# Performance work log

Measured on AMD Instinct MI355X. Metric: run time of the kernel, lower is better.

The kernel has to match this reference:

```python
import jax, jax.numpy as jnp
import numpy as np

DIM = 128
N_ROUNDS = 120


def _mlp(x, W1, b1, W2, b2, W3, b3):
    h = jax.nn.relu(x @ W1.T + b1)
    h = jax.nn.relu(h @ W2.T + b2)
    return h @ W3.T + b3


def _lstm(x, h, c, Wih, Whh, bih, bhh):
    # torch nn.LSTM gate order: i, f, g, o
    g = x @ Wih.T + h @ Whh.T + (bih + bhh)
    i, f, gg, o = jnp.split(g, 4, axis=-1)
    c2 = jax.nn.sigmoid(f) * c + jax.nn.sigmoid(i) * jnp.tanh(gg)
    h2 = jax.nn.sigmoid(o) * jnp.tanh(c2)
    return h2, c2


def setup_inputs() -> dict:
    key = jax.random.key(0)
    keys = iter(jax.random.split(key, 64))
    def w(*shape):
        return jax.random.normal(next(keys), shape, dtype=jnp.float32) * 0.05
    n_nodes, n_vars = 8000, 1000
    N = n_nodes + n_vars
    # sparse 0/1 adjacency, stored dense as in the original (adj_matrix.values)
    adj = (jax.random.uniform(next(keys), (n_nodes, N)) < 0.003).astype(jnp.float32)
    values = jax.random.randint(next(keys), (N,), 0, 2)
    inp = dict(adj=adj, values=values, n_nodes=n_nodes)
    inp.update(true_W=w(DIM, 1), true_b=w(DIM), false_W=w(DIM, 1), false_b=w(DIM))
    for p in ("cm", "pm"):
        inp.update({p + "_W1": w(DIM, DIM), p + "_b1": w(DIM),
                    p + "_W2": w(DIM, DIM), p + "_b2": w(DIM),
                    p + "_W3": w(DIM, DIM), p + "_b3": w(DIM)})
    inp.update(vv_W1=w(DIM, DIM), vv_b1=w(DIM), vv_W2=w(DIM, DIM), vv_b2=w(DIM),
               vv_W3=w(1, DIM), vv_b3=w(1))
    for p in ("vu", "nu"):
        inp.update({p + "_Wih": w(4 * DIM, DIM), p + "_Whh": w(4 * DIM, DIM),
                    p + "_bih": w(4 * DIM), p + "_bhh": w(4 * DIM)})
    return inp


def reference(adj, values, n_nodes, true_W, true_b, false_W, false_b,
              cm_W1, cm_b1, cm_W2, cm_b2, cm_W3, cm_b3,
              pm_W1, pm_b1, pm_W2, pm_b2, pm_W3, pm_b3,
              vv_W1, vv_b1, vv_W2, vv_b2, vv_W3, vv_b3,
              vu_Wih, vu_Whh, vu_bih, vu_bhh,
              nu_Wih, nu_Whh, nu_bih, nu_bhh):
    init_ts = jnp.ones((1,), jnp.float32)
    true_vec = true_W @ init_ts + true_b     # (128,)
    false_vec = false_W @ init_ts + false_b  # (128,)
    h0 = jnp.where((values == 1)[:, None], true_vec, false_vec)  # (N,128)
    c0 = jnp.zeros_like(h0)

    def step(carry, _):
        h, c = carry
        var_pre = _mlp(h, cm_W1, cm_b1, cm_W2, cm_b2, cm_W3, cm_b3)   # (N,128)
        c2p = adj @ var_pre                                           # (n_nodes,128)
        hn, cn = _lstm(c2p, h[:n_nodes], c[:n_nodes], vu_Wih, vu_Whh, vu_bih, vu_bhh)
        h = jnp.concatenate([hn, h[n_nodes:]], axis=0)
        c = jnp.concatenate([cn, c[n_nodes:]], axis=0)
        node_pre = _mlp(h[:n_nodes], pm_W1, pm_b1, pm_W2, pm_b2, pm_W3, pm_b3)
        p2c = adj.T @ node_pre                                        # (N,128)
        h, c = _lstm(p2c, h, c, nu_Wih, nu_Whh, nu_bih, nu_bhh)
        return (h, c), None

    (h, c), _ = jax.lax.scan(step, (h0, c0), None, length=N_ROUNDS)
    vote = _mlp(h[n_nodes:], vv_W1, vv_b1, vv_W2, vv_b2, vv_W3, vv_b3)  # (n_vars,1)
    return vote.squeeze(-1)
```

## Files before the change

### kernel.cpp

```cpp
#include <hip/hip_runtime.h>
#include <cstddef>
#include <cstdint>

#define DIM 128
#define NROUNDS 120
#define NNZ_CAP (1 << 20)

typedef _Float16 half8 __attribute__((ext_vector_type(8)));
typedef float f32x4 __attribute__((ext_vector_type(4)));
typedef unsigned long long u64;

__device__ __forceinline__ float sigf(float x) { return 1.f / (1.f + __expf(-x)); }
__device__ __forceinline__ float tanh_fast(float x) { return 2.f / (1.f + __expf(-2.f * x)) - 1.f; }

__global__ void count_nz_kernel(const float* __restrict__ adj, int* __restrict__ row_cnt,
                                int* __restrict__ col_cnt, int ncols) {
  int i = blockIdx.x;
  int j = blockIdx.y * blockDim.x + threadIdx.x;
  bool nz = (j < ncols) && (adj[(size_t)i * ncols + j] != 0.f);
  unsigned long long m = __ballot(nz);
  if ((threadIdx.x & 63) == 0) {
    int c = __popcll(m);
    if (c) atomicAdd(&row_cnt[i], c);
  }
  if (nz) atomicAdd(&col_cnt[j], 1);
}

__global__ void scan_kernel(const int* __restrict__ cnt, int* __restrict__ ptr, int n) {
  __shared__ int sdata[256];
  int t = threadIdx.x;
  int per = (n + 255) / 256;
  int beg = t * per;
  int end = beg + per; if (end > n) end = n;
  int local = 0;
  for (int i = beg; i < end; ++i) local += cnt[i];
  sdata[t] = local;
  __syncthreads();
  for (int off = 1; off < 256; off <<= 1) {
    int v = (t >= off) ? sdata[t - off] : 0;
    __syncthreads();
    sdata[t] += v;
    __syncthreads();
  }
  int run = sdata[t] - local;
  for (int i = beg; i < end; ++i) { ptr[i] = run; run += cnt[i]; }
  if (t == 255) ptr[n] = sdata[255];
}

__global__ __launch_bounds__(64) void fill_csr_kernel(const float* __restrict__ adj,
                                                      const int* __restrict__ row_ptr,
                                                      int* __restrict__ col_idx, int ncols) {
  int row = blockIdx.x;
  int lane = threadIdx.x;
  int base = row_ptr[row];
  int cursor = 0;
  const float* arow = adj + (size_t)row * ncols;
  for (int j0 = 0; j0 < ncols; j0 += 64) {
    int j = j0 + lane;
    bool nz = (j < ncols) && (arow[j] != 0.f);
    u64 m = __ballot(nz);
    int pre = __popcll(m & ((1ull << lane) - 1));
    if (nz) col_idx[base + cursor + pre] = j;
    cursor += __popcll(m);
  }
}

__global__ __launch_bounds__(64) void fill_csc_kernel(const float* __restrict__ adj,
                                                      const int* __restrict__ col_ptr,
                                                      int* __restrict__ row_idx,
                                                      int nrows, int ncols) {
  int c = blockIdx.x * 64 + threadIdx.x;
  if (c >= ncols) return;
  int cur = col_ptr[c];
  for (int i = 0; i < nrows; ++i) {
    if (adj[(size_t)i * ncols + c] != 0.f) row_idx[cur++] = i;
  }
}

__global__ void pack_w_kernel(const float* __restrict__ src, int out_dim,
                              _Float16* __restrict__ dh, _Float16* __restrict__ dl) {
  int idx = blockIdx.x * 256 + threadIdx.x;
  if (idx >= out_dim * DIM) return;
  int n = idx >> 7, k = idx & 127;
  float x = src[idx];
  _Float16 hi = (_Float16)x;
  _Float16 lo = (_Float16)(x - (float)hi);
  int nt = n >> 4, ks = k >> 5;
  int L = ((k >> 3) & 3) * 16 + (n & 15);
  int j = k & 7;
  int dst = ((nt * 4 + ks) * 64 + L) * 8 + j;
  dh[dst] = hi; dl[dst] = lo;
}

__global__ void init_hc_kernel(const int* __restrict__ values, const float* __restrict__ tW,
                               const float* __restrict__ tb, const float* __restrict__ fW,
                               const float* __restrict__ fb, float* __restrict__ h,
                               float* __restrict__ c, int N) {
  int idx = blockIdx.x * blockDim.x + threadIdx.x;
  if (idx >= N * DIM) return;
  int row = idx >> 7, col = idx & (DIM - 1);
  float tv = tW[col] + tb[col];
  float fv = fW[col] + fb[col];
  h[idx] = (values[row] == 1) ? tv : fv;
  c[idx] = 0.f;
}

__device__ __forceinline__ int sw_idx(int m, int k) {
  return (m << 7) + (((((k >> 3) ^ (m & 15))) << 3) | (k & 7));
}

__device__ __forceinline__ void stage_rows(const float* __restrict__ src, int M, int rb,
                                           _Float16* Sh, _Float16* Sl, int tid) {
  int r = tid >> 4, q = tid & 15;
  int row = rb + r;
  float4 v0, v1;
  if (row < M) {
    const float4* s = (const float4*)(src + (size_t)row * DIM + q * 8);
    v0 = s[0]; v1 = s[1];
  } else {
    v0.x = v0.y = v0.z = v0.w = 0.f; v1 = v0;
  }
  int a = sw_idx(r, q * 8);
  float vv[8] = {v0.x, v0.y, v0.z, v0.w, v1.x, v1.y, v1.z, v1.w};
#pragma unroll
  for (int e = 0; e < 8; ++e) {
    _Float16 hi = (_Float16)vv[e];
    Sh[a + e] = hi;
    Sl[a + e] = (_Float16)(vv[e] - (float)hi);
  }
}

__device__ __forceinline__ void gather_rows(const int* __restrict__ ptr,
                                            const int* __restrict__ nzidx,
                                            const _Float16* __restrict__ va, int M, int rb,
                                            _Float16* Xh, _Float16* Xl, int tid) {
  int r = tid >> 4, seg = tid & 15;
  int row = rb + r;
  float a[8];
#pragma unroll
  for (int e = 0; e < 8; ++e) a[e] = 0.f;
  if (row < M) {
    int s = ptr[row], e_ = ptr[row + 1];
    int p = s;
    for (; p + 4 <= e_; p += 4) {
      int i0 = nzidx[p], i1 = nzidx[p + 1], i2 = nzidx[p + 2], i3 = nzidx[p + 3];
      half8 v0 = *(const half8*)(va + (size_t)i0 * DIM + seg * 8);
      half8 v1 = *(const half8*)(va + (size_t)i1 * DIM + seg * 8);
      half8 v2 = *(const half8*)(va + (size_t)i2 * DIM + seg * 8);
      half8 v3 = *(const half8*)(va + (size_t)i3 * DIM + seg * 8);
#pragma unroll
      for (int e = 0; e < 8; ++e)
        a[e] += ((float)v0[e] + (float)v1[e]) + ((float)v2[e] + (float)v3[e]);
    }
    for (; p < e_; ++p) {
      half8 v = *(const half8*)(va + (size_t)nzidx[p] * DIM + seg * 8);
#pragma unroll
      for (int e = 0; e < 8; ++e) a[e] += (float)v[e];
    }
  }
  int aoff = sw_idx(r, seg * 8);
#pragma unroll
  for (int e = 0; e < 8; ++e) {
    _Float16 hi = (_Float16)a[e];
    Xh[aoff + e] = hi;
    Xl[aoff + e] = (_Float16)(a[e] - (float)hi);
  }
}

__device__ __forceinline__ void mfma3(f32x4& acc, half8 ah, half8 al, half8 bh, half8 bl) {
  acc = __builtin_amdgcn_mfma_f32_16x16x32_f16(ah, bh, acc, 0, 0, 0);
  acc = __builtin_amdgcn_mfma_f32_16x16x32_f16(ah, bl, acc, 0, 0, 0);
  acc = __builtin_amdgcn_mfma_f32_16x16x32_f16(al, bh, acc, 0, 0, 0);
}

__device__ __forceinline__ void mlp_layer(const _Float16* Ah_, const _Float16* Al_,
                                          const _Float16* __restrict__ Wh,
                                          const _Float16* __restrict__ Wl,
                                          const float* __restrict__ B,
                                          _Float16* Dh, _Float16* Dl, int tid) {
  int lane = tid & 63, w = tid >> 6;
  int m16 = lane & 15, quad = lane >> 4;
  float bv = B[w * 16 + m16];
  f32x4 acc[2];
  acc[0] = (f32x4){bv, bv, bv, bv};
  acc[1] = acc[0];
#pragma unroll
  for (int ks = 0; ks < 4; ++ks) {
    int boff = ((w * 4 + ks) * 64 + lane) * 8;
    half8 bh = *(const half8*)(Wh + boff);
    half8 bl = *(const half8*)(Wl + boff);
#pragma unroll
    for (int sub = 0; sub < 2; ++sub) {
      int a_off = sw_idx(sub * 16 + m16, ks * 32 + quad * 8);
      mfma3(acc[sub], *(const half8*)(Ah_ + a_off), *(const half8*)(Al_ + a_off), bh, bl);
    }
  }
#pragma unroll
  for (int sub = 0; sub < 2; ++sub)
#pragma unroll
    for (int reg = 0; reg < 4; ++reg) {
      int rl = sub * 16 + quad * 4 + reg;
      int col = w * 16 + m16;
      float x = fmaxf(acc[sub][reg], 0.f);
      _Float16 hi = (_Float16)x;
      int a = sw_idx(rl, col);
      Dh[a] = hi;
      Dl[a] = (_Float16)(x - (float)hi);
    }
  __syncthreads();
}

__device__ __forceinline__ void mlp_from_lds(
    _Float16* S0, _Float16* S1, _Float16* S2, _Float16* S3, int M, int rb,
    const _Float16* __restrict__ W1h, const _Float16* __restrict__ W1l, const float* __restrict__ b1,
    const _Float16* __restrict__ W2h, const _Float16* __restrict__ W2l, const float* __restrict__ b2,
    const _Float16* __restrict__ W3h, const _Float16* __restrict__ W3l, const float* __restrict__ b3,
    _Float16* __restrict__ out) {
  int tid = threadIdx.x;
  mlp_layer(S0, S1, W1h, W1l, b1, S2, S3, tid);
  mlp_layer(S2, S3, W2h, W2l, b2, S0, S1, tid);
  int lane = tid & 63, w = tid >> 6;
  int m16 = lane & 15, quad = lane >> 4;
  float bv = b3[w * 16 + m16];
  f32x4 acc[2];
  acc[0] = (f32x4){bv, bv, bv, bv};
  acc[1] = acc[0];
#pragma unroll
  for (int ks = 0; ks < 4; ++ks) {
    int boff = ((w * 4 + ks) * 64 + lane) * 8;
    half8 bh = *(const half8*)(W3h + boff);
    half8 bl = *(const half8*)(W3l + boff);
#pragma unroll
    for (int sub = 0; sub < 2; ++sub) {
      int a_off = sw_idx(sub * 16 + m16, ks * 32 + quad * 8);
      mfma3(acc[sub], *(const half8*)(S0 + a_off), *(const half8*)(S1 + a_off), bh, bl);
    }
  }
#pragma unroll
  for (int sub = 0; sub < 2; ++sub)
#pragma unroll
    for (int reg = 0; reg < 4; ++reg) {
      int row = rb + sub * 16 + quad * 4 + reg;
      int col = w * 16 + m16;
      if (row < M) out[(size_t)row * DIM + col] = (_Float16)acc[sub][reg];
    }
}

__global__ __launch_bounds__(512, 2) void mlp3_mfma(
    const float* __restrict__ X, int M,
    const _Float16* __restrict__ W1h, const _Float16* __restrict__ W1l, const float* __restrict__ b1,
    const _Float16* __restrict__ W2h, const _Float16* __restrict__ W2l, const float* __restrict__ b2,
    const _Float16* __restrict__ W3h, const _Float16* __restrict__ W3l, const float* __restrict__ b3,
    _Float16* __restrict__ out) {
  __shared__ _Float16 S0[4096], S1[4096], S2[4096], S3[4096];
  int tid = threadIdx.x;
  int rb = blockIdx.x << 5;
  stage_rows(X, M, rb, S0, S1, tid);
  __syncthreads();
  mlp_from_lds(S0, S1, S2, S3, M, rb, W1h, W1l, b1, W2h, W2l, b2, W3h, W3l, b3, out);
}

template <bool DO_MLP>
__global__ __launch_bounds__(512, 2) void lstm_fused(
    const int* __restrict__ ptr, const int* __restrict__ nzidx, const _Float16* __restrict__ va_in,
    float* __restrict__ hbuf, float* __restrict__ cbuf, int M,
    const _Float16* __restrict__ Wxh, const _Float16* __restrict__ Wxl,
    const _Float16* __restrict__ Whh_, const _Float16* __restrict__ Whl,
    const float* __restrict__ bih, const float* __restrict__ bhh,
    const _Float16* __restrict__ W1h, const _Float16* __restrict__ W1l, const float* __restrict__ b1,
    const _Float16* __restrict__ W2h, const _Float16* __restrict__ W2l, const float* __restrict__ b2,
    const _Float16* __restrict__ W3h, const _Float16* __restrict__ W3l, const float* __restrict__ b3,
    _Float16* __restrict__ va_out) {
  __shared__ _Float16 Xh[4096], Xl[4096], Hh[4096], Hl[4096];
  int tid = threadIdx.x;
  int rb = blockIdx.x << 5;
  stage_rows(hbuf, M, rb, Hh, Hl, tid);
  gather_rows(ptr, nzidx, va_in, M, rb, Xh, Xl, tid);
  __syncthreads();

  int lane = tid & 63, w = tid >> 6;
  int m16 = lane & 15, quad = lane >> 4;
  f32x4 acc[2][4];
#pragma unroll
  for (int g = 0; g < 4; ++g) {
    int col = g * 128 + w * 16 + m16;
    float bv = bih[col] + bhh[col];
    acc[0][g] = (f32x4){bv, bv, bv, bv};
    acc[1][g] = acc[0][g];
  }
#pragma unroll
  for (int ks = 0; ks < 4; ++ks) {
#pragma unroll
    for (int g = 0; g < 4; ++g) {
      int ct = g * 8 + w;
      int boff = ((ct * 4 + ks) * 64 + lane) * 8;
      half8 bh = *(const half8*)(Whh_ + boff);
      half8 bl = *(const half8*)(Whl + boff);
#pragma unroll
      for (int sub = 0; sub < 2; ++sub) {
        int a_off = sw_idx(sub * 16 + m16, ks * 32 + quad * 8);
        mfma3(acc[sub][g], *(const half8*)(Hh + a_off), *(const half8*)(Hl + a_off), bh, bl);
      }
    }
  }
#pragma unroll
  for (int ks = 0; ks < 4; ++ks) {
#pragma unroll
    for (int g = 0; g < 4; ++g) {
      int ct = g * 8 + w;
      int boff = ((ct * 4 + ks) * 64 + lane) * 8;
      half8 bh = *(const half8*)(Wxh + boff);
      half8 bl = *(const half8*)(Wxl + boff);
#pragma unroll
      for (int sub = 0; sub < 2; ++sub) {
        int a_off = sw_idx(sub * 16 + m16, ks * 32 + quad * 8);
        mfma3(acc[sub][g], *(const half8*)(Xh + a_off), *(const half8*)(Xl + a_off), bh, bl);
      }
    }
  }

  if (DO_MLP) __syncthreads();

#pragma unroll
  for (int sub = 0; sub < 2; ++sub)
#pragma unroll
    for (int reg = 0; reg < 4; ++reg) {
      int rl = sub * 16 + quad * 4 + reg;
      int row = rb + rl;
      int col = w * 16 + m16;
      float hn = 0.f;
      if (row < M) {
        float iv = sigf(acc[sub][0][reg]);
        float fv = sigf(acc[sub][1][reg]);
        float gv = tanh_fast(acc[sub][2][reg]);
        float ov = sigf(acc[sub][3][reg]);
        size_t o = (size_t)row * DIM + col;
        float cn = fv * cbuf[o] + iv * gv;
        cbuf[o] = cn;
        hn = ov * tanh_fast(cn);
        hbuf[o] = hn;
      }
      if (DO_MLP) {
        int a = sw_idx(rl, col);
        _Float16 hi = (_Float16)hn;
        Xh[a] = hi;
        Xl[a] = (_Float16)(hn - (float)hi);
      }
    }
  if (DO_MLP) {
    __syncthreads();
    mlp_from_lds(Xh, Xl, Hh, Hl, M, rb, W1h, W1l, b1, W2h, W2l, b2, W3h, W3l, b3, va_out);
  }
}

__device__ __forceinline__ void tile_gemm(const float* S, const float* __restrict__ W,
                                          int colB, int rowB, float acc[4][4]) {
#pragma unroll 4
  for (int kc = 0; kc < DIM; kc += 4) {
    float4 xv[4], wv[4];
#pragma unroll
    for (int r = 0; r < 4; ++r) xv[r] = *(const float4*)(S + (rowB + r) * DIM + kc);
#pragma unroll
    for (int c = 0; c < 4; ++c) wv[c] = *(const float4*)(W + (size_t)(colB + c) * DIM + kc);
#pragma unroll
    for (int r = 0; r < 4; ++r)
#pragma unroll
      for (int c = 0; c < 4; ++c)
        acc[r][c] += xv[r].x * wv[c].x + xv[r].y * wv[c].y + xv[r].z * wv[c].z + xv[r].w * wv[c].w;
  }
}

__device__ __forceinline__ void layer_lds(const float* Sin, float* Sout,
                                          const float* __restrict__ W, const float* __restrict__ B,
                                          bool relu, int colB, int rowB) {
  float acc[4][4];
#pragma unroll
  for (int r = 0; r < 4; ++r)
#pragma unroll
    for (int cc = 0; cc < 4; ++cc) acc[r][cc] = B[colB + cc];
  tile_gemm(Sin, W, colB, rowB, acc);
#pragma unroll
  for (int r = 0; r < 4; ++r) {
    float4 v;
    v.x = acc[r][0]; v.y = acc[r][1]; v.z = acc[r][2]; v.w = acc[r][3];
    if (relu) { v.x = fmaxf(v.x, 0.f); v.y = fmaxf(v.y, 0.f); v.z = fmaxf(v.z, 0.f); v.w = fmaxf(v.w, 0.f); }
    *(float4*)&Sout[(rowB + r) * DIM + colB] = v;
  }
  __syncthreads();
}

__global__ __launch_bounds__(256) void vote_kernel(
    const float* __restrict__ X, int M,
    const float* __restrict__ W1, const float* __restrict__ b1,
    const float* __restrict__ W2, const float* __restrict__ b2,
    const float* __restrict__ W3, const float* __restrict__ b3,
    float* __restrict__ out) {
  __shared__ float Xs[32 * DIM];
  __shared__ float Ys[32 * DIM];
  int tid = threadIdx.x;
  int rb = blockIdx.x * 32;
  int mrows = M - rb; if (mrows > 32) mrows = 32;
  {
    const float4* src = (const float4*)(X + (size_t)rb * DIM);
    float4* dst = (float4*)Xs;
    int nf4 = mrows * (DIM / 4);
    for (int t = tid; t < 32 * (DIM / 4); t += 256) {
      float4 v;
      if (t < nf4) v = src[t];
      else { v.x = v.y = v.z = v.w = 0.f; }
      dst[t] = v;
    }
  }
  __syncthreads();
  int tx = tid & 31, ty = tid >> 5;
  int colB = tx * 4, rowB = ty * 4;
  layer_lds(Xs, Ys, W1, b1, true, colB, rowB);
  layer_lds(Ys, Xs, W2, b2, true, colB, rowB);
  if (tid < 32) {
    int gr = rb + tid;
    if (gr < M) {
      float s = b3[0];
      for (int k = 0; k < DIM; ++k) s += Xs[tid * DIM + k] * W3[k];
      out[gr] = s;
    }
  }
}

#define SZ128 (DIM * DIM)
#define SZ512 (4 * DIM * DIM)
#define O_CM1 0
#define O_CM2 (SZ128)
#define O_CM3 (2 * SZ128)
#define O_PM1 (3 * SZ128)
#define O_PM2 (4 * SZ128)
#define O_PM3 (5 * SZ128)
#define O_VUX ((size_t)6 * SZ128)
#define O_VUH ((size_t)6 * SZ128 + SZ512)
#define O_NUX ((size_t)6 * SZ128 + 2 * SZ512)
#define O_NUH ((size_t)6 * SZ128 + 3 * SZ512)

extern "C" void kernel_launch(void* const* d_in, const int* in_sizes, int n_in,
                              void* d_out, int out_size, void* d_ws, size_t ws_size,
                              hipStream_t stream) {
  const float* adj    = (const float*)d_in[0];
  const int*   values = (const int*)d_in[1];
  const int N       = in_sizes[1];
  const int n_nodes = in_sizes[0] / N;
  const int n_vars  = N - n_nodes;

  const float* true_W  = (const float*)d_in[3];
  const float* true_b  = (const float*)d_in[4];
  const float* false_W = (const float*)d_in[5];
  const float* false_b = (const float*)d_in[6];
  const float* cm_W1 = (const float*)d_in[7];
  const float* cm_b1 = (const float*)d_in[8];
  const float* cm_W2 = (const float*)d_in[9];
  const float* cm_b2 = (const float*)d_in[10];
  const float* cm_W3 = (const float*)d_in[11];
  const float* cm_b3 = (const float*)d_in[12];
  const float* pm_W1 = (const float*)d_in[13];
  const float* pm_b1 = (const float*)d_in[14];
  const float* pm_W2 = (const float*)d_in[15];
  const float* pm_b2 = (const float*)d_in[16];
  const float* pm_W3 = (const float*)d_in[17];
  const float* pm_b3 = (const float*)d_in[18];
  const float* vv_W1 = (const float*)d_in[19];
  const float* vv_b1 = (const float*)d_in[20];
  const float* vv_W2 = (const float*)d_in[21];
  const float* vv_b2 = (const float*)d_in[22];
  const float* vv_W3 = (const float*)d_in[23];
  const float* vv_b3 = (const float*)d_in[24];
  const float* vu_Wih = (const float*)d_in[25];
  const float* vu_Whh = (const float*)d_in[26];
  const float* vu_bih = (const float*)d_in[27];
  const float* vu_bhh = (const float*)d_in[28];
  const float* nu_Wih = (const float*)d_in[29];
  const float* nu_Whh = (const float*)d_in[30];
  const float* nu_bih = (const float*)d_in[31];
  const float* nu_bhh = (const float*)d_in[32];

  uintptr_t p = (uintptr_t)d_ws;
  auto take = [&](size_t bytes) -> void* {
    uintptr_t cur = (p + 255) & ~(uintptr_t)255;
    p = cur + bytes;
    return (void*)cur;
  };
  float* h   = (float*)take((size_t)N * DIM * sizeof(float));
  float* cb  = (float*)take((size_t)N * DIM * sizeof(float));
  _Float16* va1 = (_Float16*)take((size_t)N * DIM * sizeof(_Float16));
  _Float16* va2 = (_Float16*)take((size_t)N * DIM * sizeof(_Float16));
  int* row_ptr = (int*)take((size_t)(n_nodes + 1) * sizeof(int));
  int* col_ptr = (int*)take((size_t)(N + 1) * sizeof(int));
  int* cnts    = (int*)take((size_t)(n_nodes + N) * sizeof(int));
  int* row_cnt = cnts;
  int* col_cnt = cnts + n_nodes;
  int* col_idx = (int*)take((size_t)NNZ_CAP * sizeof(int));
  int* row_idx = (int*)take((size_t)NNZ_CAP * sizeof(int));

  size_t tot_pack = (size_t)6 * SZ128 + (size_t)4 * SZ512;
  _Float16* packh = (_Float16*)take(tot_pack * sizeof(_Float16));
  _Float16* packl = (_Float16*)take(tot_pack * sizeof(_Float16));

  hipMemsetAsync(cnts, 0, (size_t)(n_nodes + N) * sizeof(int), stream);
  dim3 cgrid(n_nodes, (N + 255) / 256);
  count_nz_kernel<<<cgrid, 256, 0, stream>>>(adj, row_cnt, col_cnt, N);
  scan_kernel<<<1, 256, 0, stream>>>(row_cnt, row_ptr, n_nodes);
  scan_kernel<<<1, 256, 0, stream>>>(col_cnt, col_ptr, N);
  fill_csr_kernel<<<n_nodes, 64, 0, stream>>>(adj, row_ptr, col_idx, N);
  fill_csc_kernel<<<(N + 63) / 64, 64, 0, stream>>>(adj, col_ptr, row_idx, n_nodes, N);
  init_hc_kernel<<<(N * DIM + 255) / 256, 256, 0, stream>>>(values, true_W, true_b,
                                                            false_W, false_b, h, cb, N);

  auto pack = [&](const float* src, int out_dim, size_t o) {
    pack_w_kernel<<<(out_dim * DIM + 255) / 256, 256, 0, stream>>>(src, out_dim,
                                                                   packh + o, packl + o);
  };
  pack(cm_W1, DIM, O_CM1); pack(cm_W2, DIM, O_CM2); pack(cm_W3, DIM, O_CM3);
  pack(pm_W1, DIM, O_PM1); pack(pm_W2, DIM, O_PM2); pack(pm_W3, DIM, O_PM3);
  pack(vu_Wih, 4 * DIM, O_VUX); pack(vu_Whh, 4 * DIM, O_VUH);
  pack(nu_Wih, 4 * DIM, O_NUX); pack(nu_Whh, 4 * DIM, O_NUH);

  int tiles_N = (N + 31) / 32, tiles_n = (n_nodes + 31) / 32;

  mlp3_mfma<<<tiles_N, 512, 0, stream>>>(h, N,
      packh + O_CM1, packl + O_CM1, cm_b1,
      packh + O_CM2, packl + O_CM2, cm_b2,
      packh + O_CM3, packl + O_CM3, cm_b3, va1);

  for (int r = 0; r < NROUNDS; ++r) {
    lstm_fused<true><<<tiles_n, 512, 0, stream>>>(row_ptr, col_idx, va1, h, cb, n_nodes,
        packh + O_VUX, packl + O_VUX, packh + O_VUH, packl + O_VUH, vu_bih, vu_bhh,
        packh + O_PM1, packl + O_PM1, pm_b1,
        packh + O_PM2, packl + O_PM2, pm_b2,
        packh + O_PM3, packl + O_PM3, pm_b3, va2);
    if (r + 1 < NROUNDS) {
      lstm_fused<true><<<tiles_N, 512, 0, stream>>>(col_ptr, row_idx, va2, h, cb, N,
          packh + O_NUX, packl + O_NUX, packh + O_NUH, packl + O_NUH, nu_bih, nu_bhh,
          packh + O_CM1, packl + O_CM1, cm_b1,
          packh + O_CM2, packl + O_CM2, cm_b2,
          packh + O_CM3, packl + O_CM3, cm_b3, va1);
    } else {
      lstm_fused<false><<<tiles_N, 512, 0, stream>>>(col_ptr, row_idx, va2, h, cb, N,
          packh + O_NUX, packl + O_NUX, packh + O_NUH, packl + O_NUH, nu_bih, nu_bhh,
          packh + O_CM1, packl + O_CM1, cm_b1,
          packh + O_CM2, packl + O_CM2, cm_b2,
          packh + O_CM3, packl + O_CM3, cm_b3, va1);
    }
  }

  vote_kernel<<<(n_vars + 31) / 32, 256, 0, stream>>>(h + (size_t)n_nodes * DIM, n_vars,
      vv_W1, vv_b1, vv_W2, vv_b2, vv_W3, vv_b3, (float*)d_out);
}
```

Measured before the change: 10.86 ms.

## Drop weight low-part in split-fp16 MFMA and retile to 16-row blocks

Weights are now packed only as a single fp16 high part, so each product uses two MFMAs (A-hi*W, A-lo*W) instead of three, removing the weight low-part loads and a third of the matrix work. Blocks shrink to 16 rows and 256 threads, with each wave computing two 16-column tiles and reusing its loaded activation fragment across them. This lowers accuracy of the weight representation to plain fp16. Per-row weight fragment traffic rises because each block covers fewer rows.

```diff
diff --git a/kernel.cpp b/kernel.cpp
--- a/kernel.cpp
+++ b/kernel.cpp
@@ -78,18 +78,15 @@
 }
 
 __global__ void pack_w_kernel(const float* __restrict__ src, int out_dim,
-                              _Float16* __restrict__ dh, _Float16* __restrict__ dl) {
+                              _Float16* __restrict__ dh) {
   int idx = blockIdx.x * 256 + threadIdx.x;
   if (idx >= out_dim * DIM) return;
   int n = idx >> 7, k = idx & 127;
-  float x = src[idx];
-  _Float16 hi = (_Float16)x;
-  _Float16 lo = (_Float16)(x - (float)hi);
+  _Float16 hi = (_Float16)src[idx];
   int nt = n >> 4, ks = k >> 5;
   int L = ((k >> 3) & 3) * 16 + (n & 15);
   int j = k & 7;
-  int dst = ((nt * 4 + ks) * 64 + L) * 8 + j;
-  dh[dst] = hi; dl[dst] = lo;
+  dh[((nt * 4 + ks) * 64 + L) * 8 + j] = hi;
 }
 
 __global__ void init_hc_kernel(const int* __restrict__ values, const float* __restrict__ tW,
@@ -167,41 +164,42 @@
   }
 }
 
-__device__ __forceinline__ void mfma3(f32x4& acc, half8 ah, half8 al, half8 bh, half8 bl) {
+__device__ __forceinline__ void mfma2(f32x4& acc, half8 ah, half8 al, half8 bh) {
   acc = __builtin_amdgcn_mfma_f32_16x16x32_f16(ah, bh, acc, 0, 0, 0);
-  acc = __builtin_amdgcn_mfma_f32_16x16x32_f16(ah, bl, acc, 0, 0, 0);
   acc = __builtin_amdgcn_mfma_f32_16x16x32_f16(al, bh, acc, 0, 0, 0);
 }
 
 __device__ __forceinline__ void mlp_layer(const _Float16* Ah_, const _Float16* Al_,
                                           const _Float16* __restrict__ Wh,
-                                          const _Float16* __restrict__ Wl,
                                           const float* __restrict__ B,
                                           _Float16* Dh, _Float16* Dl, int tid) {
   int lane = tid & 63, w = tid >> 6;
   int m16 = lane & 15, quad = lane >> 4;
-  float bv = B[w * 16 + m16];
   f32x4 acc[2];
-  acc[0] = (f32x4){bv, bv, bv, bv};
-  acc[1] = acc[0];
+#pragma unroll
+  for (int c2 = 0; c2 < 2; ++c2) {
+    float bv = B[w * 32 + c2 * 16 + m16];
+    acc[c2] = (f32x4){bv, bv, bv, bv};
+  }
 #pragma unroll
   for (int ks = 0; ks < 4; ++ks) {
-    int boff = ((w * 4 + ks) * 64 + lane) * 8;
-    half8 bh = *(const half8*)(Wh + boff);
-    half8 bl = *(const half8*)(Wl + boff);
-#pragma unroll
-    for (int sub = 0; sub < 2; ++sub) {
-      int a_off = sw_idx(sub * 16 + m16, ks * 32 + quad * 8);
-      mfma3(acc[sub], *(const half8*)(Ah_ + a_off), *(const half8*)(Al_ + a_off), bh, bl);
-    }
-  }
-#pragma unroll
-  for (int sub = 0; sub < 2; ++sub)
+    int a_off = sw_idx(m16, ks * 32 + quad * 8);
+    half8 ah = *(const half8*)(Ah_ + a_off);
+    half8 al = *(const half8*)(Al_ + a_off);
+#pragma unroll
+    for (int c2 = 0; c2 < 2; ++c2) {
+      int ct = w * 2 + c2;
+      int boff = ((ct * 4 + ks) * 64 + lane) * 8;
+      mfma2(acc[c2], ah, al, *(const half8*)(Wh + boff));
+    }
+  }
+#pragma unroll
+  for (int c2 = 0; c2 < 2; ++c2)
 #pragma unroll
     for (int reg = 0; reg < 4; ++reg) {
-      int rl = sub * 16 + quad * 4 + reg;
-      int col = w * 16 + m16;
-      float x = fmaxf(acc[sub][reg], 0.f);
+      int rl = quad * 4 + reg;
+      int col = w * 32 + c2 * 16 + m16;
+      float x = fmaxf(acc[c2][reg], 0.f);
       _Float16 hi = (_Float16)x;
       int a = sw_idx(rl, col);
       Dh[a] = hi;
@@ -212,68 +210,70 @@
 
 __device__ __forceinline__ void mlp_from_lds(
     _Float16* S0, _Float16* S1, _Float16* S2, _Float16* S3, int M, int rb,
-    const _Float16* __restrict__ W1h, const _Float16* __restrict__ W1l, const float* __restrict__ b1,
-    const _Float16* __restrict__ W2h, const _Float16* __restrict__ W2l, const float* __restrict__ b2,
-    const _Float16* __restrict__ W3h, const _Float16* __restrict__ W3l, const float* __restrict__ b3,
+    const _Float16* __restrict__ W1h, const float* __restrict__ b1,
+    const _Float16* __restrict__ W2h, const float* __restrict__ b2,
+    const _Float16* __restrict__ W3h, const float* __restrict__ b3,
     _Float16* __restrict__ out) {
   int tid = threadIdx.x;
-  mlp_layer(S0, S1, W1h, W1l, b1, S2, S3, tid);
-  mlp_layer(S2, S3, W2h, W2l, b2, S0, S1, tid);
+  mlp_layer(S0, S1, W1h, b1, S2, S3, tid);
+  mlp_layer(S2, S3, W2h, b2, S0, S1, tid);
   int lane = tid & 63, w = tid >> 6;
   int m16 = lane & 15, quad = lane >> 4;
-  float bv = b3[w * 16 + m16];
   f32x4 acc[2];
-  acc[0] = (f32x4){bv, bv, bv, bv};
-  acc[1] = acc[0];
+#pragma unroll
+  for (int c2 = 0; c2 < 2; ++c2) {
+    float bv = b3[w * 32 + c2 * 16 + m16];
+    acc[c2] = (f32x4){bv, bv, bv, bv};
+  }
 #pragma unroll
   for (int ks = 0; ks < 4; ++ks) {
-    int boff = ((w * 4 + ks) * 64 + lane) * 8;
-    half8 bh = *(const half8*)(W3h + boff);
-    half8 bl = *(const half8*)(W3l + boff);
-#pragma unroll
-    for (int sub = 0; sub < 2; ++sub) {
-      int a_off = sw_idx(sub * 16 + m16, ks * 32 + quad * 8);
-      mfma3(acc[sub], *(const half8*)(S0 + a_off), *(const half8*)(S1 + a_off), bh, bl);
-    }
-  }
-#pragma unroll
-  for (int sub = 0; sub < 2; ++sub)
+    int a_off = sw_idx(m16, ks * 32 + quad * 8);
+    half8 ah = *(const half8*)(S0 + a_off);
+    half8 al = *(const half8*)(S1 + a_off);
+#pragma unroll
+    for (int c2 = 0; c2 < 2; ++c2) {
+      int ct = w * 2 + c2;
+      int boff = ((ct * 4 + ks) * 64 + lane) * 8;
+      mfma2(acc[c2], ah, al, *(const half8*)(W3h + boff));
+    }
+  }
+#pragma unroll
+  for (int c2 = 0; c2 < 2; ++c2)
 #pragma unroll
     for (int reg = 0; reg < 4; ++reg) {
-      int row = rb + sub * 16 + quad * 4 + reg;
-      int col = w * 16 + m16;
-      if (row < M) out[(size_t)row * DIM + col] = (_Float16)acc[sub][reg];
-    }
-}
-
-__global__ __launch_bounds__(512, 2) void mlp3_mfma(
+      int row = rb + quad * 4 + reg;
+      int col = w * 32 + c2 * 16 + m16;
+      if (row < M) out[(size_t)row * DIM + col] = (_Float16)acc[c2][reg];
+    }
+}
+
+__global__ __launch_bounds__(256, 4) void mlp3_mfma(
     const float* __restrict__ X, int M,
-    const _Float16* __restrict__ W1h, const _Float16* __restrict__ W1l, const float* __restrict__ b1,
-    const _Float16* __restrict__ W2h, const _Float16* __restrict__ W2l, const float* __restrict__ b2,
-    const _Float16* __restrict__ W3h, const _Float16* __restrict__ W3l, const float* __restrict__ b3,
+    const _Float16* __restrict__ W1h, const float* __restrict__ b1,
+    const _Float16* __restrict__ W2h, const float* __restrict__ b2,
+    const _Float16* __restrict__ W3h, const float* __restrict__ b3,
     _Float16* __restrict__ out) {
-  __shared__ _Float16 S0[4096], S1[4096], S2[4096], S3[4096];
+  __shared__ _Float16 S0[2048], S1[2048], S2[2048], S3[2048];
   int tid = threadIdx.x;
-  int rb = blockIdx.x << 5;
+  int rb = blockIdx.x << 4;
   stage_rows(X, M, rb, S0, S1, tid);
   __syncthreads();
-  mlp_from_lds(S0, S1, S2, S3, M, rb, W1h, W1l, b1, W2h, W2l, b2, W3h, W3l, b3, out);
+  mlp_from_lds(S0, S1, S2, S3, M, rb, W1h, b1, W2h, b2, W3h, b3, out);
 }
 
 template <bool DO_MLP>
-__global__ __launch_bounds__(512, 2) void lstm_fused(
+__global__ __launch_bounds__(256, 4) void lstm_fused(
     const int* __restrict__ ptr, const int* __restrict__ nzidx, const _Float16* __restrict__ va_in,
     float* __restrict__ hbuf, float* __restrict__ cbuf, int M,
-    const _Float16* __restrict__ Wxh, const _Float16* __restrict__ Wxl,
-    const _Float16* __restrict__ Whh_, const _Float16* __restrict__ Whl,
+    const _Float16* __restrict__ Wxh, const _Float16* __restrict__ Whh_,
     const float* __restrict__ bih, const float* __restrict__ bhh,
-    const _Float16* __restrict__ W1h, const _Float16* __restrict__ W1l, const float* __restrict__ b1,
-    const _Float16* __restrict__ W2h, const _Float16* __restrict__ W2l, const float* __restrict__ b2,
-    const _Float16* __restrict__ W3h, const _Float16* __restrict__ W3l, const float* __restrict__ b3,
+    const _Float16* __restrict__ W1h, const float* __restrict__ b1,
+    const _Float16* __restrict__ W2h, const float* __restrict__ b2,
+    const _Float16* __restrict__ W3h, const float* __restrict__ b3,
     _Float16* __restrict__ va_out) {
-  __shared__ _Float16 Xh[4096], Xl[4096], Hh[4096], Hl[4096];
+  __shared__ _Float16 Xh[2048], Xl[2048], Hh[2048], Hl[2048];
   int tid = threadIdx.x;
-  int rb = blockIdx.x << 5;
+  int rb = blockIdx.x << 4;
   stage_rows(hbuf, M, rb, Hh, Hl, tid);
   gather_rows(ptr, nzidx, va_in, M, rb, Xh, Xl, tid);
   __syncthreads();
@@ -282,58 +282,57 @@
   int m16 = lane & 15, quad = lane >> 4;
   f32x4 acc[2][4];
 #pragma unroll
-  for (int g = 0; g < 4; ++g) {
-    int col = g * 128 + w * 16 + m16;
-    float bv = bih[col] + bhh[col];
-    acc[0][g] = (f32x4){bv, bv, bv, bv};
-    acc[1][g] = acc[0][g];
-  }
+  for (int g = 0; g < 4; ++g)
+#pragma unroll
+    for (int c2 = 0; c2 < 2; ++c2) {
+      int col = g * 128 + w * 32 + c2 * 16 + m16;
+      float bv = bih[col] + bhh[col];
+      acc[c2][g] = (f32x4){bv, bv, bv, bv};
+    }
 #pragma unroll
   for (int ks = 0; ks < 4; ++ks) {
-#pragma unroll
-    for (int g = 0; g < 4; ++g) {
-      int ct = g * 8 + w;
-      int boff = ((ct * 4 + ks) * 64 + lane) * 8;
-      half8 bh = *(const half8*)(Whh_ + boff);
-      half8 bl = *(const half8*)(Whl + boff);
-#pragma unroll
-      for (int sub = 0; sub < 2; ++sub) {
-        int a_off = sw_idx(sub * 16 + m16, ks * 32 + quad * 8);
-        mfma3(acc[sub][g], *(const half8*)(Hh + a_off), *(const half8*)(Hl + a_off), bh, bl);
+    int a_off = sw_idx(m16, ks * 32 + quad * 8);
+    half8 ah = *(const half8*)(Hh + a_off);
+    half8 al = *(const half8*)(Hl + a_off);
+#pragma unroll
+    for (int g = 0; g < 4; ++g)
+#pragma unroll
+      for (int c2 = 0; c2 < 2; ++c2) {
+        int ct = g * 8 + w * 2 + c2;
+        int boff = ((ct * 4 + ks) * 64 + lane) * 8;
+        mfma2(acc[c2][g], ah, al, *(const half8*)(Whh_ + boff));
       }
-    }
   }
 #pragma unroll
   for (int ks = 0; ks < 4; ++ks) {
-#pragma unroll
-    for (int g = 0; g < 4; ++g) {
-      int ct = g * 8 + w;
-      int boff = ((ct * 4 + ks) * 64 + lane) * 8;
-      half8 bh = *(const half8*)(Wxh + boff);
-      half8 bl = *(const half8*)(Wxl + boff);
-#pragma unroll
-      for (int sub = 0; sub < 2; ++sub) {
-        int a_off = sw_idx(sub * 16 + m16, ks * 32 + quad * 8);
-        mfma3(acc[sub][g], *(const half8*)(Xh + a_off), *(const half8*)(Xl + a_off), bh, bl);
+    int a_off = sw_idx(m16, ks * 32 + quad * 8);
+    half8 ah = *(const half8*)(Xh + a_off);
+    half8 al = *(const half8*)(Xl + a_off);
+#pragma unroll
+    for (int g = 0; g < 4; ++g)
+#pragma unroll
+      for (int c2 = 0; c2 < 2; ++c2) {
+        int ct = g * 8 + w * 2 + c2;
+        int boff = ((ct * 4 + ks) * 64 + lane) * 8;
+        mfma2(acc[c2][g], ah, al, *(const half8*)(Wxh + boff));
       }
-    }
   }
 
   if (DO_MLP) __syncthreads();
 
 #pragma unroll
-  for (int sub = 0; sub < 2; ++sub)
+  for (int c2 = 0; c2 < 2; ++c2)
 #pragma unroll
     for (int reg = 0; reg < 4; ++reg) {
-      int rl = sub * 16 + quad * 4 + reg;
+      int rl = quad * 4 + reg;
       int row = rb + rl;
-      int col = w * 16 + m16;
+      int col = w * 32 + c2 * 16 + m16;
       float hn = 0.f;
       if (row < M) {
-        float iv = sigf(acc[sub][0][reg]);
-        float fv = sigf(acc[sub][1][reg]);
-        float gv = tanh_fast(acc[sub][2][reg]);
-        float ov = sigf(acc[sub][3][reg]);
+        float iv = sigf(acc[c2][0][reg]);
+        float fv = sigf(acc[c2][1][reg]);
+        float gv = tanh_fast(acc[c2][2][reg]);
+        float ov = sigf(acc[c2][3][reg]);
         size_t o = (size_t)row * DIM + col;
         float cn = fv * cbuf[o] + iv * gv;
         cbuf[o] = cn;
@@ -349,7 +348,7 @@
     }
   if (DO_MLP) {
     __syncthreads();
-    mlp_from_lds(Xh, Xl, Hh, Hl, M, rb, W1h, W1l, b1, W2h, W2l, b2, W3h, W3l, b3, va_out);
+    mlp_from_lds(Xh, Xl, Hh, Hl, M, rb, W1h, b1, W2h, b2, W3h, b3, va_out);
   }
 }
 
@@ -499,7 +498,6 @@
 
   size_t tot_pack = (size_t)6 * SZ128 + (size_t)4 * SZ512;
   _Float16* packh = (_Float16*)take(tot_pack * sizeof(_Float16));
-  _Float16* packl = (_Float16*)take(tot_pack * sizeof(_Float16));
 
   hipMemsetAsync(cnts, 0, (size_t)(n_nodes + N) * sizeof(int), stream);
   dim3 cgrid(n_nodes, (N + 255) / 256);
@@ -512,39 +510,30 @@
                                                             false_W, false_b, h, cb, N);
 
   auto pack = [&](const float* src, int out_dim, size_t o) {
-    pack_w_kernel<<<(out_dim * DIM + 255) / 256, 256, 0, stream>>>(src, out_dim,
-                                                                   packh + o, packl + o);
+    pack_w_kernel<<<(out_dim * DIM + 255) / 256, 256, 0, stream>>>(src, out_dim, packh + o);
   };
   pack(cm_W1, DIM, O_CM1); pack(cm_W2, DIM, O_CM2); pack(cm_W3, DIM, O_CM3);
   pack(pm_W1, DIM, O_PM1); pack(pm_W2, DIM, O_PM2); pack(pm_W3, DIM, O_PM3);
   pack(vu_Wih, 4 * DIM, O_VUX); pack(vu_Whh, 4 * DIM, O_VUH);
   pack(nu_Wih, 4 * DIM, O_NUX); pack(nu_Whh, 4 * DIM, O_NUH);
 
-  int tiles_N = (N + 31) / 32, tiles_n = (n_nodes + 31) / 32;
-
-  mlp3_mfma<<<tiles_N, 512, 0, stream>>>(h, N,
-      packh + O_CM1, packl + O_CM1, cm_b1,
-      packh + O_CM2, packl + O_CM2, cm_b2,
-      packh + O_CM3, packl + O_CM3, cm_b3, va1);
+  int tiles_N = (N + 15) / 16, tiles_n = (n_nodes + 15) / 16;
+
+  mlp3_mfma<<<tiles_N, 256, 0, stream>>>(h, N,
+      packh + O_CM1, cm_b1, packh + O_CM2, cm_b2, packh + O_CM3, cm_b3, va1);
 
   for (int r = 0; r < NROUNDS; ++r) {
-    lstm_fused<true><<<tiles_n, 512, 0, stream>>>(row_ptr, col_idx, va1, h, cb, n_nodes,
-        packh + O_VUX, packl + O_VUX, packh + O_VUH, packl + O_VUH, vu_bih, vu_bhh,
-        packh + O_PM1, packl + O_PM1, pm_b1,
-        packh + O_PM2, packl + O_PM2, pm_b2,
-        packh + O_PM3, packl + O_PM3, pm_b3, va2);
+    lstm_fused<true><<<tiles_n, 256, 0, stream>>>(row_ptr, col_idx, va1, h, cb, n_nodes,
+        packh + O_VUX, packh + O_VUH, vu_bih, vu_bhh,
+        packh + O_PM1, pm_b1, packh + O_PM2, pm_b2, packh + O_PM3, pm_b3, va2);
     if (r + 1 < NROUNDS) {
-      lstm_fused<true><<<tiles_N, 512, 0, stream>>>(col_ptr, row_idx, va2, h, cb, N,
-          packh + O_NUX, packl + O_NUX, packh + O_NUH, packl + O_NUH, nu_bih, nu_bhh,
-          packh + O_CM1, packl + O_CM1, cm_b1,
-          packh + O_CM2, packl + O_CM2, cm_b2,
-          packh + O_CM3, packl + O_CM3, cm_b3, va1);
+      lstm_fused<true><<<tiles_N, 256, 0, stream>>>(col_ptr, row_idx, va2, h, cb, N,
+          packh + O_NUX, packh + O_NUH, nu_bih, nu_bhh,
+          packh + O_CM1, cm_b1, packh + O_CM2, cm_b2, packh + O_CM3, cm_b3, va1);
     } else {
-      lstm_fused<false><<<tiles_N, 512, 0, stream>>>(col_ptr, row_idx, va2, h, cb, N,
-          packh + O_NUX, packl + O_NUX, packh + O_NUH, packl + O_NUH, nu_bih, nu_bhh,
-          packh + O_CM1, packl + O_CM1, cm_b1,
-          packh + O_CM2, packl + O_CM2, cm_b2,
-          packh + O_CM3, packl + O_CM3, cm_b3, va1);
+      lstm_fused<false><<<tiles_N, 256, 0, stream>>>(col_ptr, row_idx, va2, h, cb, N,
+          packh + O_NUX, packh + O_NUH, nu_bih, nu_bhh,
+          packh + O_CM1, cm_b1, packh + O_CM2, cm_b2, packh + O_CM3, cm_b3, va1);
     }
   }
 
```

Result: slower. 11.86 ms (+9.2%).
